# Kernel tuning notes

Measured on AMD Instinct MI355X. Metric: run time of the kernel, lower is better.

## Reference

```python
import jax, jax.numpy as jnp
import numpy as np

B, A, F, T = 4096, 64, 124, 8
H1, H2 = 64, 16


def setup_inputs() -> dict:
    key = jax.random.key(0)
    ks = jax.random.split(key, 10)
    x = jax.random.normal(ks[0], (B, A, F + 1), dtype=jnp.float32)
    types = jax.random.randint(ks[1], (B, A), 0, T).astype(jnp.float32)
    x = x.at[:, :, 0].set(types)  # column 0 stores atom-type index
    mask = (jax.random.uniform(ks[2], (B, A)) < 0.9).astype(jnp.float32)
    s1 = 1.0 / np.sqrt(F)
    s2 = 1.0 / np.sqrt(H1)
    s3 = 1.0 / np.sqrt(H2)
    return {
        "x_padded": x,
        "mask": mask,
        "W1": jax.random.normal(ks[3], (T, F, H1), dtype=jnp.float32) * s1,
        "b1": jax.random.normal(ks[4], (T, H1), dtype=jnp.float32) * s1,
        "W2": jax.random.normal(ks[5], (T, H1, H2), dtype=jnp.float32) * s2,
        "b2": jax.random.normal(ks[6], (T, H2), dtype=jnp.float32) * s2,
        "W3": jax.random.normal(ks[7], (T, H2, 1), dtype=jnp.float32) * s3,
        "b3": jax.random.normal(ks[8], (T, 1), dtype=jnp.float32) * s3,
    }


def reference(x_padded, mask, W1, b1, W2, b2, W3, b3):
    # x_padded: [B, A, 1+F]; mask: [B, A]
    type_idx = x_padded[:, :, 0].astype(jnp.int32)           # [B, A]
    feats = x_padded[:, :, 1:]                               # [B, A, F]
    n_types = W1.shape[0]
    # Faithful to the original: every type's subnet runs on the FULL batch
    # with non-matching atoms zero-masked (bias paths still contribute).
    type_mask = (type_idx[None, :, :] == jnp.arange(n_types)[:, None, None]).astype(feats.dtype)  # [T,B,A]
    sel = feats[None, :, :, :] * type_mask[..., None]        # [T,B,A,F]
    h = jax.nn.relu(jnp.einsum('tbaf,tfh->tbah', sel, W1) + b1[:, None, None, :])
    h = jax.nn.relu(jnp.einsum('tbah,thg->tbag', h, W2) + b2[:, None, None, :])
    o = jnp.einsum('tbag,tgo->tbao', h, W3) + b3[:, None, None, :]  # [T,B,A,1]
    per_atom = (o[..., 0] * mask[None, :, :]).sum(axis=0)   # [B, A]
    return per_atom.sum(axis=1, keepdims=True)               # [B, 1]
```

## Files before the change

kernel.cpp:

```cpp
#include <hip/hip_runtime.h>
#include <stdint.h>

#define NMOL 4096
#define APM 64
#define NATOMS (NMOL * APM)
#define NF 124
#define NT 8
#define ROWV 125

#define WS_TOTALS 0
#define WS_CURSOR 32
#define WS_DCONST 64
#define WS_TYPEBUF 128
#define WS_LIST 262400

typedef __attribute__((ext_vector_type(8))) short short8;
typedef __attribute__((ext_vector_type(4))) float floatx4;

__device__ __forceinline__ unsigned short f2bf(float f) {
    unsigned u = __builtin_bit_cast(unsigned, f);
    u += 0x7fffu + ((u >> 16) & 1u);
    return (unsigned short)(u >> 16);
}

__global__ __launch_bounds__(256) void k_zero(float* out, unsigned* totals) {
    int i = blockIdx.x * 256 + threadIdx.x;
    if (i < NMOL) out[i] = 0.0f;
    if (blockIdx.x == 0 && threadIdx.x < NT) totals[threadIdx.x] = 0u;
}

__global__ __launch_bounds__(256) void k_hist(const float* __restrict__ x,
                                              const float* __restrict__ mask,
                                              unsigned* totals,
                                              unsigned char* typebuf) {
    __shared__ unsigned hist[NT];
    int tid = threadIdx.x;
    if (tid < NT) hist[tid] = 0u;
    __syncthreads();
    int base = blockIdx.x * 1024;
    for (int i = 0; i < 4; ++i) {
        int atom = base + i * 256 + tid;
        float tf = x[(size_t)atom * ROWV];
        float m  = mask[atom];
        int t = (int)tf;
        unsigned char tb = 0xFF;
        if (m != 0.0f) { tb = (unsigned char)t; atomicAdd(&hist[t], 1u); }
        typebuf[atom] = tb;
    }
    __syncthreads();
    if (tid < NT && hist[tid]) atomicAdd(&totals[tid], hist[tid]);
}

__global__ __launch_bounds__(128) void k_setup(const float* __restrict__ b1,
                                               const float* __restrict__ W2,
                                               const float* __restrict__ b2,
                                               const float* __restrict__ W3,
                                               const float* __restrict__ b3,
                                               const unsigned* __restrict__ totals,
                                               unsigned* cursor, float* dconst) {
    __shared__ float c[NT];
    int tid = threadIdx.x;
    int t = tid >> 4, g = tid & 15;
    float acc = b2[t * 16 + g];
    for (int h = 0; h < 64; ++h) {
        float h1 = b1[t * 64 + h];
        h1 = h1 > 0.f ? h1 : 0.f;
        acc += h1 * W2[t * 1024 + h * 16 + g];
    }
    float h2 = acc > 0.f ? acc : 0.f;
    float v = h2 * W3[t * 16 + g];
    #pragma unroll
    for (int off = 1; off < 16; off <<= 1) v += __shfl_xor(v, off);
    if (g == 0) c[t] = v + b3[t];
    __syncthreads();
    if (tid == 0) {
        float tot = 0.f;
        for (int i = 0; i < NT; ++i) tot += c[i];
        unsigned run = 0;
        for (int i = 0; i < NT; ++i) {
            dconst[i] = tot - c[i];
            cursor[i] = run;
            run += totals[i];
        }
    }
}

__global__ __launch_bounds__(256) void k_scatter(const unsigned char* __restrict__ typebuf,
                                                 unsigned* cursor, unsigned* list) {
    __shared__ unsigned hist[NT], basep[NT], cur[NT];
    int tid = threadIdx.x;
    if (tid < NT) { hist[tid] = 0u; cur[tid] = 0u; }
    __syncthreads();
    int base = blockIdx.x * 1024;
    unsigned char tb[4];
    for (int i = 0; i < 4; ++i) {
        tb[i] = typebuf[base + i * 256 + tid];
        if (tb[i] != 0xFF) atomicAdd(&hist[tb[i]], 1u);
    }
    __syncthreads();
    if (tid < NT && hist[tid]) basep[tid] = atomicAdd(&cursor[tid], hist[tid]);
    __syncthreads();
    for (int i = 0; i < 4; ++i) {
        if (tb[i] != 0xFF) {
            unsigned p = basep[tb[i]] + atomicAdd(&cur[tb[i]], 1u);
            list[p] = (unsigned)(base + i * 256 + tid);
        }
    }
}

#define AS 136
#define HS 72

__global__ __launch_bounds__(256, 3) void k_mlp(const float* __restrict__ x,
                                                const float* __restrict__ W1,
                                                const float* __restrict__ b1,
                                                const float* __restrict__ W2,
                                                const float* __restrict__ b2,
                                                const float* __restrict__ W3,
                                                const float* __restrict__ b3,
                                                const unsigned* __restrict__ totals,
                                                const float* __restrict__ dconst,
                                                const unsigned* __restrict__ list,
                                                float* __restrict__ out) {
    __shared__ unsigned short sA[128 * AS];
    __shared__ unsigned short sW[64 * AS];
    __shared__ unsigned sIds[128];

    unsigned g = blockIdx.x;
    unsigned cnt[NT], start[NT];
    {
        unsigned s = 0;
        for (int i = 0; i < NT; ++i) { cnt[i] = totals[i]; start[i] = s; s += cnt[i]; }
    }
    int t = -1; unsigned tile = 0;
    {
        unsigned tl = 0;
        for (int i = 0; i < NT; ++i) {
            unsigned nt_ = (cnt[i] + 127u) >> 7;
            if (t < 0 && g < tl + nt_) { t = i; tile = g - tl; }
            tl += nt_;
        }
    }
    if (t < 0) return;

    int valid = (int)cnt[t] - (int)(tile << 7);
    if (valid > 128) valid = 128;
    unsigned rowstart = start[t] + (tile << 7);

    int tid  = threadIdx.x;
    int wv   = tid >> 6;
    int lane = tid & 63;
    int quad = lane >> 4, l15 = lane & 15;

    {
        int row = tid >> 1, half = tid & 1;
        unsigned short* dst = sA + row * AS + half * 62;
        if (row < valid) {
            unsigned atom = list[rowstart + row];
            if (half == 0) sIds[row] = atom;
            const float* src = x + (size_t)atom * ROWV + 1 + half * 62;
            #pragma unroll
            for (int j = 0; j < 62; j += 2) {
                unsigned pack = (unsigned)f2bf(src[j]) | ((unsigned)f2bf(src[j + 1]) << 16);
                *(unsigned*)(dst + j) = pack;
            }
        } else {
            #pragma unroll
            for (int j = 0; j < 62; j += 2) *(unsigned*)(dst + j) = 0u;
        }
        if (half == 1) {
            *(unsigned*)(sA + row * AS + 124) = 0u;
            *(unsigned*)(sA + row * AS + 126) = 0u;
        }
    }

    {
        const float* w1g = W1 + (size_t)t * NF * 64;
        for (int i = tid; i < NF * 64; i += 256) {
            int f = i >> 6, h = i & 63;
            sW[h * AS + f] = f2bf(w1g[i]);
        }
        int h = tid >> 2, f = 124 + (tid & 3);
        if (h < 64) sW[h * AS + f] = 0;
    }

    float b1v[4];
    #pragma unroll
    for (int n = 0; n < 4; ++n) b1v[n] = b1[t * 64 + n * 16 + l15];

    __syncthreads();

    floatx4 c1[2][4];
    #pragma unroll
    for (int m = 0; m < 2; ++m)
        #pragma unroll
        for (int n = 0; n < 4; ++n) c1[m][n] = (floatx4)0.f;

    int rowbase = wv * 32;
    #pragma unroll
    for (int ks = 0; ks < 4; ++ks) {
        int ko = ks * 32 + quad * 8;
        short8 a0 = *(const short8*)(sA + (rowbase + l15) * AS + ko);
        short8 a1 = *(const short8*)(sA + (rowbase + 16 + l15) * AS + ko);
        short8 bf[4];
        #pragma unroll
        for (int n = 0; n < 4; ++n)
            bf[n] = *(const short8*)(sW + (n * 16 + l15) * AS + ko);
        #pragma unroll
        for (int n = 0; n < 4; ++n) {
            c1[0][n] = __builtin_amdgcn_mfma_f32_16x16x32_bf16(a0, bf[n], c1[0][n], 0, 0, 0);
            c1[1][n] = __builtin_amdgcn_mfma_f32_16x16x32_bf16(a1, bf[n], c1[1][n], 0, 0, 0);
        }
    }

    __syncthreads();

    {
        const float* w2g = W2 + (size_t)t * 64 * 16;
        for (int i = tid; i < 64 * 16; i += 256) {
            int h = i >> 4, gg = i & 15;
            sW[gg * HS + h] = f2bf(w2g[i]);
        }
    }
    #pragma unroll
    for (int m = 0; m < 2; ++m)
        #pragma unroll
        for (int n = 0; n < 4; ++n) {
            int col = n * 16 + l15;
            #pragma unroll
            for (int r = 0; r < 4; ++r) {
                float v = c1[m][n][r] + b1v[n];
                v = v > 0.f ? v : 0.f;
                sA[(rowbase + m * 16 + quad * 4 + r) * HS + col] = f2bf(v);
            }
        }

    __syncthreads();

    floatx4 c2[2];
    c2[0] = (floatx4)0.f; c2[1] = (floatx4)0.f;
    #pragma unroll
    for (int ks = 0; ks < 2; ++ks) {
        int ko = ks * 32 + quad * 8;
        short8 a0 = *(const short8*)(sA + (rowbase + l15) * HS + ko);
        short8 a1 = *(const short8*)(sA + (rowbase + 16 + l15) * HS + ko);
        short8 bf = *(const short8*)(sW + l15 * HS + ko);
        c2[0] = __builtin_amdgcn_mfma_f32_16x16x32_bf16(a0, bf, c2[0], 0, 0, 0);
        c2[1] = __builtin_amdgcn_mfma_f32_16x16x32_bf16(a1, bf, c2[1], 0, 0, 0);
    }

    float b2v = b2[t * 16 + l15];
    float w3v = W3[t * 16 + l15];
    float tail = b3[t] + dconst[t];
    #pragma unroll
    for (int m = 0; m < 2; ++m) {
        float h2v[4];
        #pragma unroll
        for (int r = 0; r < 4; ++r) {
            float v = c2[m][r] + b2v;
            v = v > 0.f ? v : 0.f;
            h2v[r] = v * w3v;
        }
        #pragma unroll
        for (int off = 1; off < 16; off <<= 1)
            #pragma unroll
            for (int r = 0; r < 4; ++r) h2v[r] += __shfl_xor(h2v[r], off);
        if (l15 == 0) {
            #pragma unroll
            for (int r = 0; r < 4; ++r) {
                int trow = rowbase + m * 16 + quad * 4 + r;
                if (trow < valid) {
                    unsigned atom = sIds[trow];
                    atomicAdd(&out[atom >> 6], h2v[r] + tail);
                }
            }
        }
    }
}

extern "C" void kernel_launch(void* const* d_in, const int* in_sizes, int n_in,
                              void* d_out, int out_size, void* d_ws, size_t ws_size,
                              hipStream_t stream) {
    const float* x    = (const float*)d_in[0];
    const float* mask = (const float*)d_in[1];
    const float* W1   = (const float*)d_in[2];
    const float* b1   = (const float*)d_in[3];
    const float* W2   = (const float*)d_in[4];
    const float* b2   = (const float*)d_in[5];
    const float* W3   = (const float*)d_in[6];
    const float* b3   = (const float*)d_in[7];
    float* out = (float*)d_out;

    char* ws = (char*)d_ws;
    unsigned*       totals  = (unsigned*)(ws + WS_TOTALS);
    unsigned*       cursor  = (unsigned*)(ws + WS_CURSOR);
    float*          dconst  = (float*)(ws + WS_DCONST);
    unsigned char*  typebuf = (unsigned char*)(ws + WS_TYPEBUF);
    unsigned*       list    = (unsigned*)(ws + WS_LIST);

    k_zero<<<16, 256, 0, stream>>>(out, totals);
    k_hist<<<NATOMS / 1024, 256, 0, stream>>>(x, mask, totals, typebuf);
    k_setup<<<1, 128, 0, stream>>>(b1, W2, b2, W3, b3, totals, cursor, dconst);
    k_scatter<<<NATOMS / 1024, 256, 0, stream>>>(typebuf, cursor, list);
    k_mlp<<<2055, 256, 0, stream>>>(x, W1, b1, W2, b2, W3, b3,
                                    totals, dconst, list, out);
}
```

Measured before the change: 245.6 us.

## Pre-transpose bf16 weights once, coalesce feature gather, fold zeroing into hist

Weight conversion to bf16 and transposition now happens once in extra blocks of the histogram kernel, so each MLP block loads W1/W2 tiles with 16-byte vector copies instead of per-element strided float loads and conversions. The per-row feature gather is restructured so a whole wavefront reads one atom row with consecutive lanes, replacing the two-threads-per-row strided pattern. The output zeroing kernel is removed and merged into the histogram kernel. Global atomics on totals are replaced by per-block histogram slots reduced in the setup kernel. This adds workspace buffers and more work in the single-block setup kernel.

```diff
diff --git a/kernel.cpp b/kernel.cpp
--- a/kernel.cpp
+++ b/kernel.cpp
@@ -2,17 +2,19 @@
 #include <stdint.h>
 
 #define NMOL 4096
-#define APM 64
-#define NATOMS (NMOL * APM)
+#define NATOMS (NMOL * 64)
 #define NF 124
 #define NT 8
 #define ROWV 125
 
-#define WS_TOTALS 0
-#define WS_CURSOR 32
-#define WS_DCONST 64
-#define WS_TYPEBUF 128
-#define WS_LIST 262400
+#define WS_TOTALS  0
+#define WS_CURSOR  32
+#define WS_DCONST  64
+#define WS_HIST    128
+#define WS_TYPEBUF 8320
+#define WS_LIST    270464
+#define WS_W1T     1319040
+#define WS_W2T     1450112
 
 typedef __attribute__((ext_vector_type(8))) short short8;
 typedef __attribute__((ext_vector_type(4))) float floatx4;
@@ -23,32 +25,46 @@
     return (unsigned short)(u >> 16);
 }
 
-__global__ __launch_bounds__(256) void k_zero(float* out, unsigned* totals) {
-    int i = blockIdx.x * 256 + threadIdx.x;
-    if (i < NMOL) out[i] = 0.0f;
-    if (blockIdx.x == 0 && threadIdx.x < NT) totals[threadIdx.x] = 0u;
-}
-
 __global__ __launch_bounds__(256) void k_hist(const float* __restrict__ x,
                                               const float* __restrict__ mask,
-                                              unsigned* totals,
-                                              unsigned char* typebuf) {
-    __shared__ unsigned hist[NT];
+                                              const float* __restrict__ W1,
+                                              const float* __restrict__ W2,
+                                              unsigned* __restrict__ hist256,
+                                              unsigned char* __restrict__ typebuf,
+                                              unsigned short* __restrict__ W1T,
+                                              unsigned short* __restrict__ W2T,
+                                              float* __restrict__ out) {
     int tid = threadIdx.x;
-    if (tid < NT) hist[tid] = 0u;
-    __syncthreads();
-    int base = blockIdx.x * 1024;
-    for (int i = 0; i < 4; ++i) {
-        int atom = base + i * 256 + tid;
-        float tf = x[(size_t)atom * ROWV];
-        float m  = mask[atom];
-        int t = (int)tf;
-        unsigned char tb = 0xFF;
-        if (m != 0.0f) { tb = (unsigned char)t; atomicAdd(&hist[t], 1u); }
-        typebuf[atom] = tb;
-    }
-    __syncthreads();
-    if (tid < NT && hist[tid]) atomicAdd(&totals[tid], hist[tid]);
+    int b = blockIdx.x;
+    if (b < 256) {
+        __shared__ unsigned hist[NT];
+        if (tid < NT) hist[tid] = 0u;
+        __syncthreads();
+        int base = b * 1024;
+        for (int i = 0; i < 4; ++i) {
+            int atom = base + i * 256 + tid;
+            float tf = x[(size_t)atom * ROWV];
+            float m  = mask[atom];
+            unsigned char tb = 0xFF;
+            if (m != 0.0f) { tb = (unsigned char)(int)tf; atomicAdd(&hist[tb], 1u); }
+            typebuf[atom] = tb;
+        }
+        if (b < 16) out[b * 256 + tid] = 0.0f;
+        __syncthreads();
+        if (tid < NT) hist256[b * NT + tid] = hist[tid];
+    } else if (b < 258) {
+        for (int i = (b - 256) * 256 + tid; i < 8 * 64 * 128; i += 512) {
+            int t = i >> 13, h = (i >> 7) & 63, f = i & 127;
+            unsigned short v = 0;
+            if (f < NF) v = f2bf(W1[(size_t)t * NF * 64 + f * 64 + h]);
+            W1T[i] = v;
+        }
+    } else {
+        for (int i = tid; i < 8 * 16 * 64; i += 256) {
+            int t = i >> 10, g = (i >> 6) & 15, h = i & 63;
+            W2T[i] = f2bf(W2[(size_t)t * 1024 + h * 16 + g]);
+        }
+    }
 }
 
 __global__ __launch_bounds__(128) void k_setup(const float* __restrict__ b1,
@@ -56,31 +72,49 @@
                                                const float* __restrict__ b2,
                                                const float* __restrict__ W3,
                                                const float* __restrict__ b3,
-                                               const unsigned* __restrict__ totals,
-                                               unsigned* cursor, float* dconst) {
+                                               const unsigned* __restrict__ hist256,
+                                               unsigned* totals, unsigned* cursor,
+                                               float* dconst) {
     __shared__ float c[NT];
+    __shared__ unsigned part[16][NT];
+    __shared__ unsigned tot[NT];
     int tid = threadIdx.x;
-    int t = tid >> 4, g = tid & 15;
-    float acc = b2[t * 16 + g];
-    for (int h = 0; h < 64; ++h) {
-        float h1 = b1[t * 64 + h];
-        h1 = h1 > 0.f ? h1 : 0.f;
-        acc += h1 * W2[t * 1024 + h * 16 + g];
-    }
-    float h2 = acc > 0.f ? acc : 0.f;
-    float v = h2 * W3[t * 16 + g];
-    #pragma unroll
-    for (int off = 1; off < 16; off <<= 1) v += __shfl_xor(v, off);
-    if (g == 0) c[t] = v + b3[t];
+    {
+        int t = tid >> 4, g = tid & 15;
+        float acc = b2[t * 16 + g];
+        for (int h = 0; h < 64; ++h) {
+            float h1 = b1[t * 64 + h];
+            h1 = h1 > 0.f ? h1 : 0.f;
+            acc += h1 * W2[(size_t)t * 1024 + h * 16 + g];
+        }
+        float h2 = acc > 0.f ? acc : 0.f;
+        float v = h2 * W3[t * 16 + g];
+        #pragma unroll
+        for (int off = 1; off < 16; off <<= 1) v += __shfl_xor(v, off);
+        if (g == 0) c[t] = v + b3[t];
+    }
+    {
+        int t = tid & 7, chunk = tid >> 3;
+        unsigned s = 0;
+        for (int j = 0; j < 16; ++j) s += hist256[(chunk * 16 + j) * NT + t];
+        part[chunk][t] = s;
+    }
+    __syncthreads();
+    if (tid < NT) {
+        unsigned s = 0;
+        for (int j = 0; j < 16; ++j) s += part[j][tid];
+        tot[tid] = s;
+        totals[tid] = s;
+    }
     __syncthreads();
     if (tid == 0) {
-        float tot = 0.f;
-        for (int i = 0; i < NT; ++i) tot += c[i];
+        float T_ = 0.f;
+        for (int i = 0; i < NT; ++i) T_ += c[i];
         unsigned run = 0;
         for (int i = 0; i < NT; ++i) {
-            dconst[i] = tot - c[i];
+            dconst[i] = T_ - c[i];
             cursor[i] = run;
-            run += totals[i];
+            run += tot[i];
         }
     }
 }
@@ -112,9 +146,9 @@
 #define HS 72
 
 __global__ __launch_bounds__(256, 3) void k_mlp(const float* __restrict__ x,
-                                                const float* __restrict__ W1,
+                                                const unsigned short* __restrict__ W1T,
                                                 const float* __restrict__ b1,
-                                                const float* __restrict__ W2,
+                                                const unsigned short* __restrict__ W2T,
                                                 const float* __restrict__ b2,
                                                 const float* __restrict__ W3,
                                                 const float* __restrict__ b3,
@@ -152,36 +186,38 @@
     int lane = tid & 63;
     int quad = lane >> 4, l15 = lane & 15;
 
-    {
-        int row = tid >> 1, half = tid & 1;
-        unsigned short* dst = sA + row * AS + half * 62;
-        if (row < valid) {
-            unsigned atom = list[rowstart + row];
-            if (half == 0) sIds[row] = atom;
-            const float* src = x + (size_t)atom * ROWV + 1 + half * 62;
-            #pragma unroll
-            for (int j = 0; j < 62; j += 2) {
-                unsigned pack = (unsigned)f2bf(src[j]) | ((unsigned)f2bf(src[j + 1]) << 16);
-                *(unsigned*)(dst + j) = pack;
+    if (tid < 128) sIds[tid] = (tid < valid) ? list[rowstart + tid] : 0xFFFFFFFFu;
+
+    {
+        const unsigned short* w1g = W1T + (size_t)t * 8192;
+        #pragma unroll
+        for (int i = 0; i < 4; ++i) {
+            int c = tid * 4 + i;
+            int h = c >> 4, fp = (c & 15) * 8;
+            *(short8*)(sW + h * AS + fp) = *(const short8*)(w1g + c * 8);
+        }
+    }
+
+    {
+        unsigned ids = 0xFFFFFFFFu;
+        if (lane < 32) {
+            int r = wv * 32 + lane;
+            if (r < valid) ids = list[rowstart + r];
+        }
+        int pos = lane < 62 ? 2 * lane : 124 + 2 * (lane - 62);
+        #pragma unroll 8
+        for (int r = 0; r < 32; ++r) {
+            unsigned atom = (unsigned)__builtin_amdgcn_readlane((int)ids, r);
+            unsigned short* dst = sA + (wv * 32 + r) * AS;
+            unsigned pk = 0u;
+            if (atom != 0xFFFFFFFFu) {
+                const float* src = x + (size_t)atom * ROWV + 1;
+                float a = 0.f, bb = 0.f;
+                if (lane < 62) { a = src[2 * lane]; bb = src[2 * lane + 1]; }
+                pk = (unsigned)f2bf(a) | ((unsigned)f2bf(bb) << 16);
             }
-        } else {
-            #pragma unroll
-            for (int j = 0; j < 62; j += 2) *(unsigned*)(dst + j) = 0u;
-        }
-        if (half == 1) {
-            *(unsigned*)(sA + row * AS + 124) = 0u;
-            *(unsigned*)(sA + row * AS + 126) = 0u;
-        }
-    }
-
-    {
-        const float* w1g = W1 + (size_t)t * NF * 64;
-        for (int i = tid; i < NF * 64; i += 256) {
-            int f = i >> 6, h = i & 63;
-            sW[h * AS + f] = f2bf(w1g[i]);
-        }
-        int h = tid >> 2, f = 124 + (tid & 3);
-        if (h < 64) sW[h * AS + f] = 0;
+            *(unsigned*)(dst + pos) = pk;
+        }
     }
 
     float b1v[4];
@@ -215,12 +251,11 @@
 
     __syncthreads();
 
-    {
-        const float* w2g = W2 + (size_t)t * 64 * 16;
-        for (int i = tid; i < 64 * 16; i += 256) {
-            int h = i >> 4, gg = i & 15;
-            sW[gg * HS + h] = f2bf(w2g[i]);
-        }
+    if (tid < 128) {
+        const unsigned short* w2g = W2T + (size_t)t * 1024;
+        int c = tid;
+        int gg = c >> 3, hp = (c & 7) * 8;
+        *(short8*)(sW + gg * HS + hp) = *(const short8*)(w2g + c * 8);
     }
     #pragma unroll
     for (int m = 0; m < 2; ++m)
@@ -295,13 +330,15 @@
     unsigned*       totals  = (unsigned*)(ws + WS_TOTALS);
     unsigned*       cursor  = (unsigned*)(ws + WS_CURSOR);
     float*          dconst  = (float*)(ws + WS_DCONST);
+    unsigned*       hist256 = (unsigned*)(ws + WS_HIST);
     unsigned char*  typebuf = (unsigned char*)(ws + WS_TYPEBUF);
     unsigned*       list    = (unsigned*)(ws + WS_LIST);
-
-    k_zero<<<16, 256, 0, stream>>>(out, totals);
-    k_hist<<<NATOMS / 1024, 256, 0, stream>>>(x, mask, totals, typebuf);
-    k_setup<<<1, 128, 0, stream>>>(b1, W2, b2, W3, b3, totals, cursor, dconst);
+    unsigned short* W1T     = (unsigned short*)(ws + WS_W1T);
+    unsigned short* W2T     = (unsigned short*)(ws + WS_W2T);
+
+    k_hist<<<259, 256, 0, stream>>>(x, mask, W1, W2, hist256, typebuf, W1T, W2T, out);
+    k_setup<<<1, 128, 0, stream>>>(b1, W2, b2, W3, b3, hist256, totals, cursor, dconst);
     k_scatter<<<NATOMS / 1024, 256, 0, stream>>>(typebuf, cursor, list);
-    k_mlp<<<2055, 256, 0, stream>>>(x, W1, b1, W2, b2, W3, b3,
+    k_mlp<<<2055, 256, 0, stream>>>(x, W1T, b1, W2T, b2, W3, b3,
                                     totals, dconst, list, out);
 }
```

Measured after the change: 290.6 us. +18.3%, slower.

## Fuse histogram/scatter into per-molecule pack kernel with pre-swizzled bf16 rows

Applied to the files above, without the earlier changes.

Replaces the hist/setup/scatter pipeline with a single pack kernel. Each block loads one molecule's rows coalesced into LDS, assigns slots in fixed-capacity per-type buckets through atomic cursors, and writes XOR-swizzled bf16 rows to a packed buffer. Weights are pre-converted to bf16 in swizzled and transposed form by the setup kernel. The MLP kernel then fills LDS with direct global_load_lds copies instead of gathering and converting strided fp32 rows. The cost is an extra packed intermediate written to and read from memory, plus a fixed 4096-block grid with many early-exit blocks; a type count above CAP (65536) would overflow its bucket.

```diff
diff --git a/kernel.cpp b/kernel.cpp
--- a/kernel.cpp
+++ b/kernel.cpp
@@ -2,20 +2,22 @@
 #include <stdint.h>
 
 #define NMOL 4096
-#define APM 64
-#define NATOMS (NMOL * APM)
+#define NATOMS (NMOL * 64)
 #define NF 124
 #define NT 8
 #define ROWV 125
-
-#define WS_TOTALS 0
-#define WS_CURSOR 32
-#define WS_DCONST 64
-#define WS_TYPEBUF 128
-#define WS_LIST 262400
+#define CAP 65536
+
+#define WS_CURSOR   0
+#define WS_DCONST   64
+#define WS_W2T      1024
+#define WS_W1S      18432
+#define WS_IDS      1048576
+#define WS_PACKED   4194304
 
 typedef __attribute__((ext_vector_type(8))) short short8;
 typedef __attribute__((ext_vector_type(4))) float floatx4;
+typedef __attribute__((ext_vector_type(4))) unsigned int uint4v;
 
 __device__ __forceinline__ unsigned short f2bf(float f) {
     unsigned u = __builtin_bit_cast(unsigned, f);
@@ -23,166 +25,173 @@
     return (unsigned short)(u >> 16);
 }
 
-__global__ __launch_bounds__(256) void k_zero(float* out, unsigned* totals) {
-    int i = blockIdx.x * 256 + threadIdx.x;
-    if (i < NMOL) out[i] = 0.0f;
-    if (blockIdx.x == 0 && threadIdx.x < NT) totals[threadIdx.x] = 0u;
-}
-
-__global__ __launch_bounds__(256) void k_hist(const float* __restrict__ x,
-                                              const float* __restrict__ mask,
-                                              unsigned* totals,
-                                              unsigned char* typebuf) {
-    __shared__ unsigned hist[NT];
-    int tid = threadIdx.x;
-    if (tid < NT) hist[tid] = 0u;
-    __syncthreads();
-    int base = blockIdx.x * 1024;
-    for (int i = 0; i < 4; ++i) {
-        int atom = base + i * 256 + tid;
-        float tf = x[(size_t)atom * ROWV];
-        float m  = mask[atom];
-        int t = (int)tf;
-        unsigned char tb = 0xFF;
-        if (m != 0.0f) { tb = (unsigned char)t; atomicAdd(&hist[t], 1u); }
-        typebuf[atom] = tb;
-    }
-    __syncthreads();
-    if (tid < NT && hist[tid]) atomicAdd(&totals[tid], hist[tid]);
-}
-
-__global__ __launch_bounds__(128) void k_setup(const float* __restrict__ b1,
+__device__ __forceinline__ void ld_lds16(const void* g, void* lds) {
+    __builtin_amdgcn_global_load_lds(
+        (const __attribute__((address_space(1))) unsigned int*)g,
+        (__attribute__((address_space(3))) unsigned int*)lds, 16, 0, 0);
+}
+
+__global__ __launch_bounds__(256) void k_setup(const float* __restrict__ W1,
+                                               const float* __restrict__ b1,
                                                const float* __restrict__ W2,
                                                const float* __restrict__ b2,
                                                const float* __restrict__ W3,
                                                const float* __restrict__ b3,
-                                               const unsigned* __restrict__ totals,
-                                               unsigned* cursor, float* dconst) {
-    __shared__ float c[NT];
-    int tid = threadIdx.x;
-    int t = tid >> 4, g = tid & 15;
-    float acc = b2[t * 16 + g];
-    for (int h = 0; h < 64; ++h) {
-        float h1 = b1[t * 64 + h];
-        h1 = h1 > 0.f ? h1 : 0.f;
-        acc += h1 * W2[t * 1024 + h * 16 + g];
-    }
-    float h2 = acc > 0.f ? acc : 0.f;
-    float v = h2 * W3[t * 16 + g];
-    #pragma unroll
-    for (int off = 1; off < 16; off <<= 1) v += __shfl_xor(v, off);
-    if (g == 0) c[t] = v + b3[t];
-    __syncthreads();
-    if (tid == 0) {
-        float tot = 0.f;
-        for (int i = 0; i < NT; ++i) tot += c[i];
-        unsigned run = 0;
-        for (int i = 0; i < NT; ++i) {
-            dconst[i] = tot - c[i];
-            cursor[i] = run;
-            run += totals[i];
-        }
-    }
-}
-
-__global__ __launch_bounds__(256) void k_scatter(const unsigned char* __restrict__ typebuf,
-                                                 unsigned* cursor, unsigned* list) {
-    __shared__ unsigned hist[NT], basep[NT], cur[NT];
-    int tid = threadIdx.x;
-    if (tid < NT) { hist[tid] = 0u; cur[tid] = 0u; }
-    __syncthreads();
-    int base = blockIdx.x * 1024;
-    unsigned char tb[4];
-    for (int i = 0; i < 4; ++i) {
-        tb[i] = typebuf[base + i * 256 + tid];
-        if (tb[i] != 0xFF) atomicAdd(&hist[tb[i]], 1u);
-    }
-    __syncthreads();
-    if (tid < NT && hist[tid]) basep[tid] = atomicAdd(&cursor[tid], hist[tid]);
-    __syncthreads();
-    for (int i = 0; i < 4; ++i) {
-        if (tb[i] != 0xFF) {
-            unsigned p = basep[tb[i]] + atomicAdd(&cur[tb[i]], 1u);
-            list[p] = (unsigned)(base + i * 256 + tid);
-        }
-    }
-}
-
-#define AS 136
+                                               unsigned* __restrict__ cursor,
+                                               float* __restrict__ dconst,
+                                               unsigned short* __restrict__ W1S,
+                                               unsigned short* __restrict__ W2T,
+                                               float* __restrict__ out) {
+    int tid = threadIdx.x, b = blockIdx.x;
+    if (b == 0) {
+        __shared__ float c[NT];
+        if (tid < 128) {
+            int t = tid >> 4, g = tid & 15;
+            float acc = b2[t * 16 + g];
+            for (int h = 0; h < 64; ++h) {
+                float h1 = b1[t * 64 + h];
+                h1 = h1 > 0.f ? h1 : 0.f;
+                acc += h1 * W2[(size_t)t * 1024 + h * 16 + g];
+            }
+            float h2 = acc > 0.f ? acc : 0.f;
+            float v = h2 * W3[t * 16 + g];
+            #pragma unroll
+            for (int off = 1; off < 16; off <<= 1) v += __shfl_xor(v, off);
+            if (g == 0) c[t] = v + b3[t];
+        }
+        if (tid < NT) cursor[tid] = (unsigned)(tid * CAP);
+        __syncthreads();
+        if (tid == 0) {
+            float T_ = 0.f;
+            for (int i = 0; i < NT; ++i) T_ += c[i];
+            for (int i = 0; i < NT; ++i) dconst[i] = T_ - c[i];
+        }
+    } else if (b <= 8) {
+        int t = b - 1;
+        const float* w1g = W1 + (size_t)t * NF * 64;
+        unsigned short* dst = W1S + (size_t)t * 8192;
+        for (int id = tid; id < 1024; id += 256) {
+            int h = id >> 4, cc = id & 15;
+            unsigned u[4];
+            #pragma unroll
+            for (int j = 0; j < 4; ++j) {
+                int f0 = cc * 8 + 2 * j;
+                unsigned short lo = (f0 < NF)     ? f2bf(w1g[f0 * 64 + h])       : (unsigned short)0;
+                unsigned short hi = (f0 + 1 < NF) ? f2bf(w1g[(f0 + 1) * 64 + h]) : (unsigned short)0;
+                u[j] = (unsigned)lo | ((unsigned)hi << 16);
+            }
+            int p = cc ^ (h & 15);
+            *(uint4v*)(dst + h * 128 + p * 8) = (uint4v){u[0], u[1], u[2], u[3]};
+        }
+    } else if (b == 9) {
+        for (int i = tid; i < 8 * 16 * 64; i += 256) {
+            int t = i >> 10, g = (i >> 6) & 15, h = i & 63;
+            W2T[i] = f2bf(W2[(size_t)t * 1024 + h * 16 + g]);
+        }
+    } else {
+        out[(b - 10) * 256 + tid] = 0.0f;
+    }
+}
+
+__global__ __launch_bounds__(256, 4) void k_pack(const float* __restrict__ x,
+                                                 const float* __restrict__ mask,
+                                                 unsigned* __restrict__ cursor,
+                                                 unsigned* __restrict__ ids,
+                                                 unsigned short* __restrict__ packed) {
+    __shared__ __align__(16) float sRaw[64 * ROWV];
+    __shared__ unsigned sHist[NT], sBase[NT];
+    __shared__ int sDest[64];
+    int tid = threadIdx.x, b = blockIdx.x;
+    if (tid < NT) sHist[tid] = 0u;
+    {
+        const uint4v* xs = (const uint4v*)(x + (size_t)b * 64 * ROWV);
+        uint4v* sr = (uint4v*)sRaw;
+        for (int i = tid; i < 2000; i += 256) sr[i] = xs[i];
+    }
+    float m = 0.f;
+    if (tid < 64) m = mask[b * 64 + tid];
+    __syncthreads();
+    int t = 0, rank = -1;
+    bool kept = false;
+    if (tid < 64) {
+        t = (int)sRaw[tid * ROWV];
+        kept = (m != 0.f);
+        if (kept) rank = (int)atomicAdd(&sHist[t], 1u);
+    }
+    __syncthreads();
+    if (tid < NT && sHist[tid]) sBase[tid] = atomicAdd(&cursor[tid], sHist[tid]);
+    __syncthreads();
+    if (tid < 64) {
+        int d = kept ? (int)(sBase[t] + (unsigned)rank) : -1;
+        sDest[tid] = d;
+        if (kept) ids[d] = (unsigned)b;
+    }
+    __syncthreads();
+    for (int s = tid; s < 512; s += 256) {
+        int r = s >> 3, k = s & 7;
+        int d = sDest[r];
+        if (d < 0) continue;
+        const float* src = sRaw + r * ROWV + 1;
+        unsigned u[8];
+        #pragma unroll
+        for (int j = 0; j < 8; ++j) {
+            int c0 = k * 16 + 2 * j;
+            float a  = (c0 < NF)     ? src[c0]     : 0.f;
+            float bb = (c0 + 1 < NF) ? src[c0 + 1] : 0.f;
+            u[j] = (unsigned)f2bf(a) | ((unsigned)f2bf(bb) << 16);
+        }
+        int skey = d & 15;
+        uint4v* drow = (uint4v*)(packed + (size_t)d * 128);
+        drow[(2 * k) ^ skey]     = (uint4v){u[0], u[1], u[2], u[3]};
+        drow[(2 * k + 1) ^ skey] = (uint4v){u[4], u[5], u[6], u[7]};
+    }
+}
+
 #define HS 72
 
-__global__ __launch_bounds__(256, 3) void k_mlp(const float* __restrict__ x,
-                                                const float* __restrict__ W1,
+__global__ __launch_bounds__(256, 3) void k_mlp(const unsigned short* __restrict__ packed,
+                                                const unsigned short* __restrict__ W1S,
                                                 const float* __restrict__ b1,
-                                                const float* __restrict__ W2,
+                                                const unsigned short* __restrict__ W2T,
                                                 const float* __restrict__ b2,
                                                 const float* __restrict__ W3,
                                                 const float* __restrict__ b3,
-                                                const unsigned* __restrict__ totals,
+                                                const unsigned* __restrict__ cursor,
                                                 const float* __restrict__ dconst,
-                                                const unsigned* __restrict__ list,
+                                                const unsigned* __restrict__ ids,
                                                 float* __restrict__ out) {
-    __shared__ unsigned short sA[128 * AS];
-    __shared__ unsigned short sW[64 * AS];
+    __shared__ unsigned short sA[128 * 128];
+    __shared__ unsigned short sW[64 * 128];
     __shared__ unsigned sIds[128];
 
-    unsigned g = blockIdx.x;
-    unsigned cnt[NT], start[NT];
-    {
-        unsigned s = 0;
-        for (int i = 0; i < NT; ++i) { cnt[i] = totals[i]; start[i] = s; s += cnt[i]; }
-    }
-    int t = -1; unsigned tile = 0;
-    {
-        unsigned tl = 0;
-        for (int i = 0; i < NT; ++i) {
-            unsigned nt_ = (cnt[i] + 127u) >> 7;
-            if (t < 0 && g < tl + nt_) { t = i; tile = g - tl; }
-            tl += nt_;
-        }
-    }
-    if (t < 0) return;
-
-    int valid = (int)cnt[t] - (int)(tile << 7);
+    int t = blockIdx.x >> 9;
+    int tile = blockIdx.x & 511;
+    int cnt = (int)(cursor[t] - (unsigned)(t * CAP));
+    int valid = cnt - (tile << 7);
+    if (valid <= 0) return;
     if (valid > 128) valid = 128;
-    unsigned rowstart = start[t] + (tile << 7);
 
     int tid  = threadIdx.x;
     int wv   = tid >> 6;
     int lane = tid & 63;
     int quad = lane >> 4, l15 = lane & 15;
+    int rowstart = t * CAP + (tile << 7);
 
     {
-        int row = tid >> 1, half = tid & 1;
-        unsigned short* dst = sA + row * AS + half * 62;
-        if (row < valid) {
-            unsigned atom = list[rowstart + row];
-            if (half == 0) sIds[row] = atom;
-            const float* src = x + (size_t)atom * ROWV + 1 + half * 62;
-            #pragma unroll
-            for (int j = 0; j < 62; j += 2) {
-                unsigned pack = (unsigned)f2bf(src[j]) | ((unsigned)f2bf(src[j + 1]) << 16);
-                *(unsigned*)(dst + j) = pack;
-            }
-        } else {
-            #pragma unroll
-            for (int j = 0; j < 62; j += 2) *(unsigned*)(dst + j) = 0u;
-        }
-        if (half == 1) {
-            *(unsigned*)(sA + row * AS + 124) = 0u;
-            *(unsigned*)(sA + row * AS + 126) = 0u;
-        }
-    }
-
-    {
-        const float* w1g = W1 + (size_t)t * NF * 64;
-        for (int i = tid; i < NF * 64; i += 256) {
-            int f = i >> 6, h = i & 63;
-            sW[h * AS + f] = f2bf(w1g[i]);
-        }
-        int h = tid >> 2, f = 124 + (tid & 3);
-        if (h < 64) sW[h * AS + f] = 0;
-    }
+        const char* aseg = (const char*)packed + (size_t)rowstart * 256;
+        #pragma unroll
+        for (int i = 0; i < 8; ++i) {
+            int off = (wv * 8 + i) * 1024;
+            ld_lds16(aseg + off + lane * 16, (char*)sA + off);
+        }
+        const char* wseg = (const char*)W1S + (size_t)t * 16384;
+        #pragma unroll
+        for (int i = 0; i < 4; ++i) {
+            int off = (wv * 4 + i) * 1024;
+            ld_lds16(wseg + off + lane * 16, (char*)sW + off);
+        }
+    }
+    if (tid < 128) sIds[tid] = ids[rowstart + tid];
 
     float b1v[4];
     #pragma unroll
@@ -199,13 +208,13 @@
     int rowbase = wv * 32;
     #pragma unroll
     for (int ks = 0; ks < 4; ++ks) {
-        int ko = ks * 32 + quad * 8;
-        short8 a0 = *(const short8*)(sA + (rowbase + l15) * AS + ko);
-        short8 a1 = *(const short8*)(sA + (rowbase + 16 + l15) * AS + ko);
+        int p = ((ks * 4 + quad) ^ l15) * 8;
+        short8 a0 = *(const short8*)(sA + (rowbase + l15) * 128 + p);
+        short8 a1 = *(const short8*)(sA + (rowbase + 16 + l15) * 128 + p);
         short8 bf[4];
         #pragma unroll
         for (int n = 0; n < 4; ++n)
-            bf[n] = *(const short8*)(sW + (n * 16 + l15) * AS + ko);
+            bf[n] = *(const short8*)(sW + (n * 16 + l15) * 128 + p);
         #pragma unroll
         for (int n = 0; n < 4; ++n) {
             c1[0][n] = __builtin_amdgcn_mfma_f32_16x16x32_bf16(a0, bf[n], c1[0][n], 0, 0, 0);
@@ -215,12 +224,10 @@
 
     __syncthreads();
 
-    {
-        const float* w2g = W2 + (size_t)t * 64 * 16;
-        for (int i = tid; i < 64 * 16; i += 256) {
-            int h = i >> 4, gg = i & 15;
-            sW[gg * HS + h] = f2bf(w2g[i]);
-        }
+    if (tid < 128) {
+        const unsigned short* w2g = W2T + (size_t)t * 1024;
+        int gg = tid >> 3, hp = (tid & 7) * 8;
+        *(short8*)(sW + gg * HS + hp) = *(const short8*)(w2g + tid * 8);
     }
     #pragma unroll
     for (int m = 0; m < 2; ++m)
@@ -270,8 +277,7 @@
             for (int r = 0; r < 4; ++r) {
                 int trow = rowbase + m * 16 + quad * 4 + r;
                 if (trow < valid) {
-                    unsigned atom = sIds[trow];
-                    atomicAdd(&out[atom >> 6], h2v[r] + tail);
+                    atomicAdd(&out[sIds[trow]], h2v[r] + tail);
                 }
             }
         }
@@ -292,16 +298,15 @@
     float* out = (float*)d_out;
 
     char* ws = (char*)d_ws;
-    unsigned*       totals  = (unsigned*)(ws + WS_TOTALS);
-    unsigned*       cursor  = (unsigned*)(ws + WS_CURSOR);
-    float*          dconst  = (float*)(ws + WS_DCONST);
-    unsigned char*  typebuf = (unsigned char*)(ws + WS_TYPEBUF);
-    unsigned*       list    = (unsigned*)(ws + WS_LIST);
-
-    k_zero<<<16, 256, 0, stream>>>(out, totals);
-    k_hist<<<NATOMS / 1024, 256, 0, stream>>>(x, mask, totals, typebuf);
-    k_setup<<<1, 128, 0, stream>>>(b1, W2, b2, W3, b3, totals, cursor, dconst);
-    k_scatter<<<NATOMS / 1024, 256, 0, stream>>>(typebuf, cursor, list);
-    k_mlp<<<2055, 256, 0, stream>>>(x, W1, b1, W2, b2, W3, b3,
-                                    totals, dconst, list, out);
-}
+    unsigned*       cursor = (unsigned*)(ws + WS_CURSOR);
+    float*          dconst = (float*)(ws + WS_DCONST);
+    unsigned short* W2T    = (unsigned short*)(ws + WS_W2T);
+    unsigned short* W1S    = (unsigned short*)(ws + WS_W1S);
+    unsigned*       ids    = (unsigned*)(ws + WS_IDS);
+    unsigned short* packed = (unsigned short*)(ws + WS_PACKED);
+
+    k_setup<<<26, 256, 0, stream>>>(W1, b1, W2, b2, W3, b3, cursor, dconst, W1S, W2T, out);
+    k_pack<<<NMOL, 256, 0, stream>>>(x, mask, cursor, ids, packed);
+    k_mlp<<<NT * (CAP / 128), 256, 0, stream>>>(packed, W1S, b1, W2T, b2, W3, b3,
+                                                cursor, dconst, ids, out);
+}
```

Result: slower. 267.8 us (+9.1%).
